# Performance work log

Hardware: AMD Instinct MI355X
Metric: run time of the kernel (lower is better)

Reference implementation:

```python
import jax, jax.numpy as jnp
import numpy as np

# Normalized sobel kernels (kornia normalize_kernel2d: divide by abs-sum = 8)
_SOBEL = np.array([
    [[-1., 0., 1.], [-2., 0., 2.], [-1., 0., 1.]],   # d/dx
    [[-1., -2., -1.], [0., 0., 0.], [1., 2., 1.]],   # d/dy
], dtype=np.float32) / 8.0
_EPS = 1e-6


def _rgb_to_grayscale(x):
    # kornia weights; x: [B,3,H,W] -> [B,1,H,W]
    return 0.299 * x[:, 0:1] + 0.587 * x[:, 1:2] + 0.114 * x[:, 2:3]


def _sobel_edges(x):
    gray = _rgb_to_grayscale(x)
    # replicate padding of 1 (kornia spatial_gradient uses replicate)
    p = jnp.pad(gray, ((0, 0), (0, 0), (1, 1), (1, 1)), mode='edge')
    k = jnp.asarray(_SOBEL)[:, None]  # [2,1,3,3] OIHW
    g = jax.lax.conv_general_dilated(
        p, k, window_strides=(1, 1), padding='VALID',
        dimension_numbers=('NCHW', 'OIHW', 'NCHW'))  # [B,2,H,W]
    # gradient magnitude: sqrt(gx^2 + gy^2 + eps)
    return jnp.sqrt(jnp.sum(g * g, axis=1, keepdims=True) + _EPS)  # [B,1,H,W]


def setup_inputs() -> dict:
    key = jax.random.key(0)
    k1, k2 = jax.random.split(key)
    shape = (16, 3, 512, 512)
    prediction = jax.random.uniform(k1, shape, dtype=jnp.float32)
    target = jax.random.uniform(k2, shape, dtype=jnp.float32)
    return {"prediction": prediction, "target": target}


def reference(prediction, target):
    # forward runs under torch.no_grad() in the original module
    pe = jax.lax.stop_gradient(_sobel_edges(prediction))
    te = jax.lax.stop_gradient(_sobel_edges(target))
    return jnp.mean(jnp.abs(pe - te))  # l1_loss, mean reduction
```

## Files before the change

### kernel.cpp

```cpp
#include <hip/hip_runtime.h>


constexpr int B = 16;
constexpr int H = 512;
constexpr int W = 512;
constexpr int TH = 32;
constexpr int TW = 64;
constexpr int HROWS = TH + 2;
constexpr int LSTRIDE = 72;
constexpr int NTHREADS = 256;
constexpr int TILES_W = W / TW;
constexpr int TILES_H = H / TH;
constexpr int TILES_PER_IMG = TILES_W * TILES_H;
constexpr int NBLOCKS = B * TILES_PER_IMG;
constexpr float EPS = 1e-6f;

__device__ __forceinline__ float4 ldg4(const float* p) {
    return *reinterpret_cast<const float4*>(p);
}

__device__ __forceinline__ float4 gray4(float4 r, float4 g, float4 b) {
    float4 o;
    o.x = 0.299f * r.x + 0.587f * g.x + 0.114f * b.x;
    o.y = 0.299f * r.y + 0.587f * g.y + 0.114f * b.y;
    o.z = 0.299f * r.z + 0.587f * g.z + 0.114f * b.z;
    o.w = 0.299f * r.w + 0.587f * g.w + 0.114f * b.w;
    return o;
}

__global__ __launch_bounds__(NTHREADS, 4) void edge_loss_kernel(
    const float* __restrict__ pred,
    const float* __restrict__ targ,
    float* __restrict__ partial)
{
    __shared__ alignas(16) float sp[HROWS][LSTRIDE];
    __shared__ alignas(16) float st[HROWS][LSTRIDE];

    const int bid = blockIdx.x;
    const int b   = bid / TILES_PER_IMG;
    const int t   = bid % TILES_PER_IMG;
    const int th0 = (t / TILES_W) * TH;
    const int tw0 = (t % TILES_W) * TW;
    const int tid = threadIdx.x;
    const size_t plane = (size_t)H * W;

    const float* __restrict__ p0 = pred + (size_t)b * 3 * plane;
    const float* __restrict__ p1 = p0 + plane;
    const float* __restrict__ p2 = p0 + 2 * plane;
    const float* __restrict__ t0 = targ + (size_t)b * 3 * plane;
    const float* __restrict__ t1 = t0 + plane;
    const float* __restrict__ t2 = t0 + 2 * plane;

    const int rowA = tid >> 4, kA = tid & 15;
    const int gB = tid + 256;
    const int rowB = gB >> 4, kB = gB & 15;
    const int offA = (min(max(th0 - 1 + rowA, 0), H - 1)) * W + tw0 + 4 * kA;
    const int offB = (min(max(th0 - 1 + rowB, 0), H - 1)) * W + tw0 + 4 * kB;

    const float4 Apr = ldg4(p0 + offA), Apg = ldg4(p1 + offA), Apb = ldg4(p2 + offA);
    const float4 Atr = ldg4(t0 + offA), Atg = ldg4(t1 + offA), Atb = ldg4(t2 + offA);
    const float4 Bpr = ldg4(p0 + offB), Bpg = ldg4(p1 + offB), Bpb = ldg4(p2 + offB);
    const float4 Btr = ldg4(t0 + offB), Btg = ldg4(t1 + offB), Btb = ldg4(t2 + offB);

    float hv0 = 0.f, hv1 = 0.f, hv2 = 0.f;
    int hrow = 0, hside = 0, himg = 0;
    if (tid < 4 * HROWS) {
        himg = tid & 1;
        const int rr = tid >> 1;
        hside = rr >= HROWS;
        hrow  = hside ? rr - HROWS : rr;
        const int grow = min(max(th0 - 1 + hrow, 0), H - 1);
        const int gcol = hside ? min(tw0 + TW, W - 1) : max(tw0 - 1, 0);
        const float* ip = (himg ? t0 : p0) + (size_t)grow * W + gcol;
        hv0 = ip[0]; hv1 = ip[plane]; hv2 = ip[2 * plane];
    }

    float4 Cpr, Cpg, Cpb, Ctr, Ctg, Ctb;
    int rowC = 0, kC = 0;
    if (tid < 32) {
        const int gC = tid + 512;
        rowC = gC >> 4; kC = gC & 15;
        const int offC = (min(max(th0 - 1 + rowC, 0), H - 1)) * W + tw0 + 4 * kC;
        Cpr = ldg4(p0 + offC); Cpg = ldg4(p1 + offC); Cpb = ldg4(p2 + offC);
        Ctr = ldg4(t0 + offC); Ctg = ldg4(t1 + offC); Ctb = ldg4(t2 + offC);
    }

    *reinterpret_cast<float4*>(&sp[rowA][4 + 4 * kA]) = gray4(Apr, Apg, Apb);
    *reinterpret_cast<float4*>(&st[rowA][4 + 4 * kA]) = gray4(Atr, Atg, Atb);
    *reinterpret_cast<float4*>(&sp[rowB][4 + 4 * kB]) = gray4(Bpr, Bpg, Bpb);
    *reinterpret_cast<float4*>(&st[rowB][4 + 4 * kB]) = gray4(Btr, Btg, Btb);

    if (tid < 4 * HROWS) {
        const float v = 0.299f * hv0 + 0.587f * hv1 + 0.114f * hv2;
        float (*dst)[LSTRIDE] = himg ? st : sp;
        dst[hrow][hside ? 68 : 3] = v;
    }
    if (tid < 32) {
        *reinterpret_cast<float4*>(&sp[rowC][4 + 4 * kC]) = gray4(Cpr, Cpg, Cpb);
        *reinterpret_cast<float4*>(&st[rowC][4 + 4 * kC]) = gray4(Ctr, Ctg, Ctb);
    }

    __syncthreads();

    const int lw = tid & 63;
    const int q  = tid >> 6;
    const int r0 = q * 8;
    const int c0 = lw + 3, c1 = lw + 4, c2 = lw + 5;

    float pa0 = sp[r0][c0],     pa1 = sp[r0][c1],     pa2 = sp[r0][c2];
    float pb0 = sp[r0 + 1][c0], pb1 = sp[r0 + 1][c1], pb2 = sp[r0 + 1][c2];
    float ta0 = st[r0][c0],     ta1 = st[r0][c1],     ta2 = st[r0][c2];
    float tb0 = st[r0 + 1][c0], tb1 = st[r0 + 1][c1], tb2 = st[r0 + 1][c2];

    float acc = 0.0f;
    #pragma unroll
    for (int r = 0; r < 8; ++r) {
        const int hr = r0 + r + 2;
        const float pc0 = sp[hr][c0], pc1 = sp[hr][c1], pc2 = sp[hr][c2];
        const float tc0 = st[hr][c0], tc1 = st[hr][c1], tc2 = st[hr][c2];

        float gx = ((pa2 - pa0) + 2.0f * (pb2 - pb0) + (pc2 - pc0)) * 0.125f;
        float gy = ((pc0 - pa0) + 2.0f * (pc1 - pa1) + (pc2 - pa2)) * 0.125f;
        const float pe = sqrtf(gx * gx + gy * gy + EPS);

        float hx = ((ta2 - ta0) + 2.0f * (tb2 - tb0) + (tc2 - tc0)) * 0.125f;
        float hy = ((tc0 - ta0) + 2.0f * (tc1 - ta1) + (tc2 - ta2)) * 0.125f;
        const float te = sqrtf(hx * hx + hy * hy + EPS);

        acc += fabsf(pe - te);

        pa0 = pb0; pa1 = pb1; pa2 = pb2;
        pb0 = pc0; pb1 = pc1; pb2 = pc2;
        ta0 = tb0; ta1 = tb1; ta2 = tb2;
        tb0 = tc0; tb1 = tc1; tb2 = tc2;
    }

    #pragma unroll
    for (int off = 32; off > 0; off >>= 1)
        acc += __shfl_down(acc, off);

    __shared__ float wsum[NTHREADS / 64];
    if ((tid & 63) == 0) wsum[tid >> 6] = acc;
    __syncthreads();

    if (tid == 0) {
        partial[bid] = wsum[0] + wsum[1] + wsum[2] + wsum[3];
    }
}

__global__ __launch_bounds__(256) void reduce_kernel(
    const float* __restrict__ partial,
    float* __restrict__ out)
{
    const int tid = threadIdx.x;
    float acc = 0.0f;
    #pragma unroll
    for (int i = 0; i < NBLOCKS / 256; ++i)
        acc += partial[tid + i * 256];

    #pragma unroll
    for (int off = 32; off > 0; off >>= 1)
        acc += __shfl_down(acc, off);

    __shared__ float wsum[4];
    if ((tid & 63) == 0) wsum[tid >> 6] = acc;
    __syncthreads();

    if (tid == 0) {
        const float s = wsum[0] + wsum[1] + wsum[2] + wsum[3];
        out[0] = s * (1.0f / (float)((size_t)B * H * W));
    }
}

extern "C" void kernel_launch(void* const* d_in, const int* in_sizes, int n_in,
                              void* d_out, int out_size, void* d_ws, size_t ws_size,
                              hipStream_t stream) {
    const float* pred = (const float*)d_in[0];
    const float* targ = (const float*)d_in[1];
    float* out = (float*)d_out;
    float* partial = (float*)d_ws;

    edge_loss_kernel<<<NBLOCKS, NTHREADS, 0, stream>>>(pred, targ, partial);
    reduce_kernel<<<1, 256, 0, stream>>>(partial, out);
}
```

Measured before the change: 123.1 us.

## Process two vertical tiles per block with register-prefetched second tile

Each block now handles two vertically adjacent 32x64 tiles instead of one, halving the grid. The second tile's global loads are issued into registers before computing the first tile, so load latency can overlap with the stencil compute. The cost is higher register pressure from holding a full stage of float4 loads (risking spills or lower occupancy under the launch bound) and fewer blocks in flight.

Result: no change. 124.9 us (+1.5%).

```diff
diff --git a/kernel.cpp b/kernel.cpp
--- a/kernel.cpp
+++ b/kernel.cpp
@@ -9,10 +9,10 @@
 constexpr int HROWS = TH + 2;
 constexpr int LSTRIDE = 72;
 constexpr int NTHREADS = 256;
-constexpr int TILES_W = W / TW;
-constexpr int TILES_H = H / TH;
-constexpr int TILES_PER_IMG = TILES_W * TILES_H;
-constexpr int NBLOCKS = B * TILES_PER_IMG;
+constexpr int PAIRS_W = W / TW;
+constexpr int PAIRS_H = H / (2 * TH);
+constexpr int PAIRS_PER_IMG = PAIRS_W * PAIRS_H;
+constexpr int NBLOCKS = B * PAIRS_PER_IMG;
 constexpr float EPS = 1e-6f;
 
 __device__ __forceinline__ float4 ldg4(const float* p) {
@@ -28,6 +28,119 @@
     return o;
 }
 
+struct Stage {
+    float4 Apr, Apg, Apb, Atr, Atg, Atb;
+    float4 Bpr, Bpg, Bpb, Btr, Btg, Btb;
+    float  hv0, hv1, hv2;
+    float4 Cpr, Cpg, Cpb, Ctr, Ctg, Ctb;
+};
+
+__device__ __forceinline__ Stage issue_stage(
+    const float* __restrict__ p0, const float* __restrict__ p1, const float* __restrict__ p2,
+    const float* __restrict__ t0, const float* __restrict__ t1, const float* __restrict__ t2,
+    int th0, int tw0, int tid, size_t plane)
+{
+    Stage S;
+    S.hv0 = S.hv1 = S.hv2 = 0.0f;
+
+    const int rowA = tid >> 4, kA = tid & 15;
+    const int gB = tid + 256;
+    const int rowB = gB >> 4, kB = gB & 15;
+    const int offA = (min(max(th0 - 1 + rowA, 0), H - 1)) * W + tw0 + 4 * kA;
+    const int offB = (min(max(th0 - 1 + rowB, 0), H - 1)) * W + tw0 + 4 * kB;
+
+    S.Apr = ldg4(p0 + offA); S.Apg = ldg4(p1 + offA); S.Apb = ldg4(p2 + offA);
+    S.Atr = ldg4(t0 + offA); S.Atg = ldg4(t1 + offA); S.Atb = ldg4(t2 + offA);
+    S.Bpr = ldg4(p0 + offB); S.Bpg = ldg4(p1 + offB); S.Bpb = ldg4(p2 + offB);
+    S.Btr = ldg4(t0 + offB); S.Btg = ldg4(t1 + offB); S.Btb = ldg4(t2 + offB);
+
+    if (tid < 4 * HROWS) {
+        const int img  = tid & 1;
+        const int rr   = tid >> 1;
+        const int side = rr >= HROWS;
+        const int row  = side ? rr - HROWS : rr;
+        const int grow = min(max(th0 - 1 + row, 0), H - 1);
+        const int gcol = side ? min(tw0 + TW, W - 1) : max(tw0 - 1, 0);
+        const float* ip = (img ? t0 : p0) + (size_t)grow * W + gcol;
+        S.hv0 = ip[0]; S.hv1 = ip[plane]; S.hv2 = ip[2 * plane];
+    }
+    if (tid < 32) {
+        const int gC = tid + 512;
+        const int rowC = gC >> 4, kC = gC & 15;
+        const int offC = (min(max(th0 - 1 + rowC, 0), H - 1)) * W + tw0 + 4 * kC;
+        S.Cpr = ldg4(p0 + offC); S.Cpg = ldg4(p1 + offC); S.Cpb = ldg4(p2 + offC);
+        S.Ctr = ldg4(t0 + offC); S.Ctg = ldg4(t1 + offC); S.Ctb = ldg4(t2 + offC);
+    }
+    return S;
+}
+
+__device__ __forceinline__ void consume_stage(
+    const Stage& S, float sp[HROWS][LSTRIDE], float st[HROWS][LSTRIDE], int tid)
+{
+    const int rowA = tid >> 4, kA = tid & 15;
+    const int gB = tid + 256;
+    const int rowB = gB >> 4, kB = gB & 15;
+
+    *reinterpret_cast<float4*>(&sp[rowA][4 + 4 * kA]) = gray4(S.Apr, S.Apg, S.Apb);
+    *reinterpret_cast<float4*>(&st[rowA][4 + 4 * kA]) = gray4(S.Atr, S.Atg, S.Atb);
+    *reinterpret_cast<float4*>(&sp[rowB][4 + 4 * kB]) = gray4(S.Bpr, S.Bpg, S.Bpb);
+    *reinterpret_cast<float4*>(&st[rowB][4 + 4 * kB]) = gray4(S.Btr, S.Btg, S.Btb);
+
+    if (tid < 4 * HROWS) {
+        const int img  = tid & 1;
+        const int rr   = tid >> 1;
+        const int side = rr >= HROWS;
+        const int row  = side ? rr - HROWS : rr;
+        const float v = 0.299f * S.hv0 + 0.587f * S.hv1 + 0.114f * S.hv2;
+        float (*dst)[LSTRIDE] = img ? st : sp;
+        dst[row][side ? 68 : 3] = v;
+    }
+    if (tid < 32) {
+        const int gC = tid + 512;
+        const int rowC = gC >> 4, kC = gC & 15;
+        *reinterpret_cast<float4*>(&sp[rowC][4 + 4 * kC]) = gray4(S.Cpr, S.Cpg, S.Cpb);
+        *reinterpret_cast<float4*>(&st[rowC][4 + 4 * kC]) = gray4(S.Ctr, S.Ctg, S.Ctb);
+    }
+}
+
+__device__ __forceinline__ float compute_tile(
+    const float sp[HROWS][LSTRIDE], const float st[HROWS][LSTRIDE], int tid)
+{
+    const int lw = tid & 63;
+    const int q  = tid >> 6;
+    const int r0 = q * 8;
+    const int c0 = lw + 3, c1 = lw + 4, c2 = lw + 5;
+
+    float pa0 = sp[r0][c0],     pa1 = sp[r0][c1],     pa2 = sp[r0][c2];
+    float pb0 = sp[r0 + 1][c0], pb1 = sp[r0 + 1][c1], pb2 = sp[r0 + 1][c2];
+    float ta0 = st[r0][c0],     ta1 = st[r0][c1],     ta2 = st[r0][c2];
+    float tb0 = st[r0 + 1][c0], tb1 = st[r0 + 1][c1], tb2 = st[r0 + 1][c2];
+
+    float acc = 0.0f;
+    #pragma unroll
+    for (int r = 0; r < 8; ++r) {
+        const int hr = r0 + r + 2;
+        const float pc0 = sp[hr][c0], pc1 = sp[hr][c1], pc2 = sp[hr][c2];
+        const float tc0 = st[hr][c0], tc1 = st[hr][c1], tc2 = st[hr][c2];
+
+        float gx = ((pa2 - pa0) + 2.0f * (pb2 - pb0) + (pc2 - pc0)) * 0.125f;
+        float gy = ((pc0 - pa0) + 2.0f * (pc1 - pa1) + (pc2 - pa2)) * 0.125f;
+        const float pe = sqrtf(gx * gx + gy * gy + EPS);
+
+        float hx = ((ta2 - ta0) + 2.0f * (tb2 - tb0) + (tc2 - tc0)) * 0.125f;
+        float hy = ((tc0 - ta0) + 2.0f * (tc1 - ta1) + (tc2 - ta2)) * 0.125f;
+        const float te = sqrtf(hx * hx + hy * hy + EPS);
+
+        acc += fabsf(pe - te);
+
+        pa0 = pb0; pa1 = pb1; pa2 = pb2;
+        pb0 = pc0; pb1 = pc1; pb2 = pc2;
+        ta0 = tb0; ta1 = tb1; ta2 = tb2;
+        tb0 = tc0; tb1 = tc1; tb2 = tc2;
+    }
+    return acc;
+}
+
 __global__ __launch_bounds__(NTHREADS, 4) void edge_loss_kernel(
     const float* __restrict__ pred,
     const float* __restrict__ targ,
@@ -37,10 +150,10 @@
     __shared__ alignas(16) float st[HROWS][LSTRIDE];
 
     const int bid = blockIdx.x;
-    const int b   = bid / TILES_PER_IMG;
-    const int t   = bid % TILES_PER_IMG;
-    const int th0 = (t / TILES_W) * TH;
-    const int tw0 = (t % TILES_W) * TW;
+    const int b   = bid / PAIRS_PER_IMG;
+    const int t   = bid % PAIRS_PER_IMG;
+    const int th0 = (t / PAIRS_W) * (2 * TH);
+    const int tw0 = (t % PAIRS_W) * TW;
     const int tid = threadIdx.x;
     const size_t plane = (size_t)H * W;
 
@@ -51,89 +164,19 @@
     const float* __restrict__ t1 = t0 + plane;
     const float* __restrict__ t2 = t0 + 2 * plane;
 
-    const int rowA = tid >> 4, kA = tid & 15;
-    const int gB = tid + 256;
-    const int rowB = gB >> 4, kB = gB & 15;
-    const int offA = (min(max(th0 - 1 + rowA, 0), H - 1)) * W + tw0 + 4 * kA;
-    const int offB = (min(max(th0 - 1 + rowB, 0), H - 1)) * W + tw0 + 4 * kB;
-
-    const float4 Apr = ldg4(p0 + offA), Apg = ldg4(p1 + offA), Apb = ldg4(p2 + offA);
-    const float4 Atr = ldg4(t0 + offA), Atg = ldg4(t1 + offA), Atb = ldg4(t2 + offA);
-    const float4 Bpr = ldg4(p0 + offB), Bpg = ldg4(p1 + offB), Bpb = ldg4(p2 + offB);
-    const float4 Btr = ldg4(t0 + offB), Btg = ldg4(t1 + offB), Btb = ldg4(t2 + offB);
-
-    float hv0 = 0.f, hv1 = 0.f, hv2 = 0.f;
-    int hrow = 0, hside = 0, himg = 0;
-    if (tid < 4 * HROWS) {
-        himg = tid & 1;
-        const int rr = tid >> 1;
-        hside = rr >= HROWS;
-        hrow  = hside ? rr - HROWS : rr;
-        const int grow = min(max(th0 - 1 + hrow, 0), H - 1);
-        const int gcol = hside ? min(tw0 + TW, W - 1) : max(tw0 - 1, 0);
-        const float* ip = (himg ? t0 : p0) + (size_t)grow * W + gcol;
-        hv0 = ip[0]; hv1 = ip[plane]; hv2 = ip[2 * plane];
-    }
-
-    float4 Cpr, Cpg, Cpb, Ctr, Ctg, Ctb;
-    int rowC = 0, kC = 0;
-    if (tid < 32) {
-        const int gC = tid + 512;
-        rowC = gC >> 4; kC = gC & 15;
-        const int offC = (min(max(th0 - 1 + rowC, 0), H - 1)) * W + tw0 + 4 * kC;
-        Cpr = ldg4(p0 + offC); Cpg = ldg4(p1 + offC); Cpb = ldg4(p2 + offC);
-        Ctr = ldg4(t0 + offC); Ctg = ldg4(t1 + offC); Ctb = ldg4(t2 + offC);
-    }
-
-    *reinterpret_cast<float4*>(&sp[rowA][4 + 4 * kA]) = gray4(Apr, Apg, Apb);
-    *reinterpret_cast<float4*>(&st[rowA][4 + 4 * kA]) = gray4(Atr, Atg, Atb);
-    *reinterpret_cast<float4*>(&sp[rowB][4 + 4 * kB]) = gray4(Bpr, Bpg, Bpb);
-    *reinterpret_cast<float4*>(&st[rowB][4 + 4 * kB]) = gray4(Btr, Btg, Btb);
-
-    if (tid < 4 * HROWS) {
-        const float v = 0.299f * hv0 + 0.587f * hv1 + 0.114f * hv2;
-        float (*dst)[LSTRIDE] = himg ? st : sp;
-        dst[hrow][hside ? 68 : 3] = v;
-    }
-    if (tid < 32) {
-        *reinterpret_cast<float4*>(&sp[rowC][4 + 4 * kC]) = gray4(Cpr, Cpg, Cpb);
-        *reinterpret_cast<float4*>(&st[rowC][4 + 4 * kC]) = gray4(Ctr, Ctg, Ctb);
-    }
-
-    __syncthreads();
-
-    const int lw = tid & 63;
-    const int q  = tid >> 6;
-    const int r0 = q * 8;
-    const int c0 = lw + 3, c1 = lw + 4, c2 = lw + 5;
-
-    float pa0 = sp[r0][c0],     pa1 = sp[r0][c1],     pa2 = sp[r0][c2];
-    float pb0 = sp[r0 + 1][c0], pb1 = sp[r0 + 1][c1], pb2 = sp[r0 + 1][c2];
-    float ta0 = st[r0][c0],     ta1 = st[r0][c1],     ta2 = st[r0][c2];
-    float tb0 = st[r0 + 1][c0], tb1 = st[r0 + 1][c1], tb2 = st[r0 + 1][c2];
-
-    float acc = 0.0f;
-    #pragma unroll
-    for (int r = 0; r < 8; ++r) {
-        const int hr = r0 + r + 2;
-        const float pc0 = sp[hr][c0], pc1 = sp[hr][c1], pc2 = sp[hr][c2];
-        const float tc0 = st[hr][c0], tc1 = st[hr][c1], tc2 = st[hr][c2];
-
-        float gx = ((pa2 - pa0) + 2.0f * (pb2 - pb0) + (pc2 - pc0)) * 0.125f;
-        float gy = ((pc0 - pa0) + 2.0f * (pc1 - pa1) + (pc2 - pa2)) * 0.125f;
-        const float pe = sqrtf(gx * gx + gy * gy + EPS);
-
-        float hx = ((ta2 - ta0) + 2.0f * (tb2 - tb0) + (tc2 - tc0)) * 0.125f;
-        float hy = ((tc0 - ta0) + 2.0f * (tc1 - ta1) + (tc2 - ta2)) * 0.125f;
-        const float te = sqrtf(hx * hx + hy * hy + EPS);
-
-        acc += fabsf(pe - te);
-
-        pa0 = pb0; pa1 = pb1; pa2 = pb2;
-        pb0 = pc0; pb1 = pc1; pb2 = pc2;
-        ta0 = tb0; ta1 = tb1; ta2 = tb2;
-        tb0 = tc0; tb1 = tc1; tb2 = tc2;
-    }
+    Stage S0 = issue_stage(p0, p1, p2, t0, t1, t2, th0, tw0, tid, plane);
+    consume_stage(S0, sp, st, tid);
+    __syncthreads();
+
+    Stage S1 = issue_stage(p0, p1, p2, t0, t1, t2, th0 + TH, tw0, tid, plane);
+
+    float acc = compute_tile(sp, st, tid);
+    __syncthreads();
+
+    consume_stage(S1, sp, st, tid);
+    __syncthreads();
+
+    acc += compute_tile(sp, st, tid);
 
     #pragma unroll
     for (int off = 32; off > 0; off >>= 1)
```
